# Kernel optimization log

Hardware: AMD Instinct MI355X
Metric: run time of the kernel (lower is better)

The kernel has to match this reference:

```python
import jax, jax.numpy as jnp
import numpy as np

LOG2 = float(np.log(2.0))

def ssp(x):
    # shifted softplus: log(0.5*exp(x) + 0.5)
    return jax.nn.softplus(x) - LOG2


def setup_inputs() -> dict:
    B, A, N = 8, 512, 64
    n_atom, n_spatial, n_filters = 256, 128, 256
    n_ang_feat = 2 * 2 * 2 * 8 * 2  # 2*n_zetas*2*n_angular*n_zetas = 128
    key = jax.random.key(0)
    ks = jax.random.split(key, 16)
    f32 = jnp.float32
    inp = {
        'x': jax.random.normal(ks[0], (B, A, n_atom), f32),
        'r_ij': jax.random.uniform(ks[1], (B, A, N), f32) * 6.0,  # some beyond cutoff=5
        'f_ij': jax.random.normal(ks[2], (B, A, N, n_spatial), f32),
        'G_i': jax.random.normal(ks[3], (B, A, n_ang_feat), f32),
        'neighbor_mask': jnp.ones((B, A, N), f32),
        'neighbors': jax.random.randint(ks[4], (B, A, N), 0, A),
        # CFConv params: in2f (no bias), filter MLP, f2out
        'W_in2f': jax.random.normal(ks[5], (n_atom, n_filters), f32) * (n_atom ** -0.5),
        'W1': jax.random.normal(ks[6], (n_spatial, n_filters), f32) * (n_spatial ** -0.5),
        'b1': jnp.zeros((n_filters,), f32),
        'W2': jax.random.normal(ks[7], (n_filters, n_filters), f32) * (n_filters ** -0.5),
        'b2': jnp.zeros((n_filters,), f32),
        'W_f2out': jax.random.normal(ks[8], (n_filters, n_atom), f32) * (n_filters ** -0.5),
        'b_f2out': jnp.zeros((n_atom,), f32),
        # post-cfconv dense and angular dense (no bias)
        'W_dense': jax.random.normal(ks[9], (n_atom, n_atom), f32) * (n_atom ** -0.5),
        'b_dense': jnp.zeros((n_atom,), f32),
        'W_ang': jax.random.normal(ks[10], (n_ang_feat, n_atom), f32) * (n_ang_feat ** -0.5),
    }
    return inp


def reference(x, r_ij, f_ij, G_i, neighbor_mask, neighbors,
              W_in2f, W1, b1, W2, b2, W_f2out, b_f2out,
              W_dense, b_dense, W_ang):
    cutoff = 5.0
    # filter-generating MLP on distance expansion: [B,A,N,n_filters]
    W = ssp(jnp.einsum('bans,sf->banf', f_ij, W1) + b1)
    W = jnp.einsum('banf,fg->bang', W, W2) + b2
    # hard cutoff mask on distances
    C = (r_ij <= cutoff).astype(W.dtype)
    W = W * C[..., None]
    # in2f projection then neighbor gather
    xf = jnp.einsum('bad,df->baf', x, W_in2f)  # [B,A,F]
    B, A, F = xf.shape
    N = neighbors.shape[-1]
    y = jnp.take_along_axis(xf, neighbors.reshape(B, A * N, 1), axis=1)
    y = y.reshape(B, A, N, F)
    # elementwise filter, mask padded neighbors, sum-aggregate over neighbors
    y = (y * W * neighbor_mask[..., None]).sum(axis=2)  # [B,A,F]
    v_rad = jnp.einsum('baf,fd->bad', y, W_f2out) + b_f2out
    v_rad = jnp.einsum('bad,de->bae', v_rad, W_dense) + b_dense
    v_ang = jnp.einsum('bag,gd->bad', G_i, W_ang)
    return ssp(v_rad + v_ang)
```

## Files before the change

kernel.cpp:

```cpp
#include <hip/hip_runtime.h>


typedef __bf16 bf16x8 __attribute__((ext_vector_type(8)));
typedef float f32x4 __attribute__((ext_vector_type(4)));
typedef unsigned short u16;

#define LDA 136
#define LDH 264

__device__ __forceinline__ float b2f(u16 u) {
  union { float f; unsigned int i; } v; v.i = ((unsigned int)u) << 16; return v.f;
}
__device__ __forceinline__ u16 f2b(float f) {
  unsigned int u = __builtin_bit_cast(unsigned int, f);
  return (u16)((u + 0x7fffu + ((u >> 16) & 1u)) >> 16);
}
__device__ __forceinline__ float sspf(float x) {
  float t = __expf(-fabsf(x));
  return fmaxf(x, 0.0f) + __logf(1.0f + t) - 0.6931471805599453f;
}
__device__ __forceinline__ bf16x8 ldfrag(const u16* p) {
  return __builtin_bit_cast(bf16x8, *(const uint4*)p);
}
__device__ __forceinline__ float ldsc(const u16* p, bool fm, size_t i) {
  return fm ? ((const float*)p)[i] : b2f(p[i]);
}
__device__ __forceinline__ void cvt8_store(u16* dst, const float* s) {
  float4 a = *(const float4*)s, b = *(const float4*)(s + 4);
  uint4 r;
  r.x = (unsigned)f2b(a.x) | ((unsigned)f2b(a.y) << 16);
  r.y = (unsigned)f2b(a.z) | ((unsigned)f2b(a.w) << 16);
  r.z = (unsigned)f2b(b.x) | ((unsigned)f2b(b.y) << 16);
  r.w = (unsigned)f2b(b.z) | ((unsigned)f2b(b.w) << 16);
  *(uint4*)dst = r;
}
__device__ __forceinline__ bf16x8 ldfragW(const u16* W, bool fm, int k0, int col, int quad) {
  union { u16 s[8]; bf16x8 v; } r;
  if (fm) {
    const float* W32 = (const float*)W;
#pragma unroll
    for (int j = 0; j < 8; j++) r.s[j] = f2b(W32[(size_t)(k0 + quad * 8 + j) * 256 + col]);
  } else {
#pragma unroll
    for (int j = 0; j < 8; j++) r.s[j] = W[(size_t)(k0 + quad * 8 + j) * 256 + col];
  }
  return r.v;
}

__global__ __launch_bounds__(256) void k1_xf(
    const u16* __restrict__ x, const u16* __restrict__ Win,
    const u16* __restrict__ nm, u16* __restrict__ xf) {
  __shared__ __align__(16) u16 sX[64 * LDH];
  bool fm = (nm[0] == 0);
  int bid = blockIdx.x, tid = threadIdx.x;
  int w = tid >> 6, lane = tid & 63, quad = lane >> 4, l16 = lane & 15;
  if (fm) {
    const float* src = (const float*)x + (size_t)bid * 16384;
#pragma unroll
    for (int i = 0; i < 8; i++) {
      int c = tid + 256 * i;
      cvt8_store(sX + (c >> 5) * LDH + (c & 31) * 8, src + c * 8);
    }
  } else {
    const u16* src = x + (size_t)bid * 16384;
#pragma unroll
    for (int i = 0; i < 8; i++) {
      int c = tid + 256 * i;
      *(uint4*)(sX + (c >> 5) * LDH + (c & 31) * 8) = *(const uint4*)(src + c * 8);
    }
  }
  __syncthreads();
  f32x4 zero = {0.f, 0.f, 0.f, 0.f};
  f32x4 acc[4][4];
#pragma unroll
  for (int mt = 0; mt < 4; mt++)
#pragma unroll
    for (int ct = 0; ct < 4; ct++) acc[mt][ct] = zero;
#pragma unroll
  for (int q = 0; q < 8; q++) {
    bf16x8 af[4], bf[4];
#pragma unroll
    for (int mt = 0; mt < 4; mt++)
      af[mt] = ldfrag(sX + (mt * 16 + l16) * LDH + q * 32 + quad * 8);
#pragma unroll
    for (int ct = 0; ct < 4; ct++)
      bf[ct] = ldfragW(Win, fm, q * 32, (w * 4 + ct) * 16 + l16, quad);
#pragma unroll
    for (int mt = 0; mt < 4; mt++)
#pragma unroll
      for (int ct = 0; ct < 4; ct++)
        acc[mt][ct] = __builtin_amdgcn_mfma_f32_16x16x32_bf16(af[mt], bf[ct], acc[mt][ct], 0, 0, 0);
  }
#pragma unroll
  for (int ct = 0; ct < 4; ct++) {
    int f = w * 64 + ct * 16 + l16;
#pragma unroll
    for (int mt = 0; mt < 4; mt++)
#pragma unroll
      for (int r = 0; r < 4; r++) {
        int m = bid * 64 + mt * 16 + quad * 4 + r;
        xf[(size_t)m * 256 + f] = f2b(acc[mt][ct][r]);
      }
  }
}

__global__ __launch_bounds__(256) void pack5(
    const u16* __restrict__ W1, const u16* __restrict__ W2, const u16* __restrict__ Wf,
    const u16* __restrict__ Wd, const u16* __restrict__ Wa,
    const u16* __restrict__ nm, u16* __restrict__ dst) {
  bool fm = (nm[0] == 0);
  int bid = blockIdx.x;
  const u16* W; u16* Wp; int ksh;
  if (bid < 128)       { W = W1; Wp = dst;          ksh = 2; }
  else if (bid < 384)  { W = W2; Wp = dst + 32768;  ksh = 3; bid -= 128; }
  else if (bid < 640)  { W = Wf; Wp = dst + 98304;  ksh = 3; bid -= 384; }
  else if (bid < 896)  { W = Wd; Wp = dst + 163840; ksh = 3; bid -= 640; }
  else                 { W = Wa; Wp = dst + 229376; ksh = 2; bid -= 896; }
  int tid = bid * 256 + threadIdx.x;
  int j = tid & 7, lane = (tid >> 3) & 63, rest = tid >> 9;
  int q = rest & ((1 << ksh) - 1), c = rest >> ksh;
  int row = q * 32 + (lane >> 4) * 8 + j, col = c * 16 + (lane & 15);
  float v = ldsc(W, fm, (size_t)row * 256 + col);
  Wp[tid] = f2b(v);
}

__global__ __launch_bounds__(256, 2) void k2_main(
    u16* __restrict__ fij, const u16* __restrict__ rij, const u16* __restrict__ nm,
    const int* __restrict__ nbr, const u16* __restrict__ b1, const u16* __restrict__ b2,
    const u16* __restrict__ packed, const u16* __restrict__ xf) {
  __shared__ __align__(16) u16 uA[64 * LDH];
  __shared__ __align__(16) u16 sH[64 * LDH];
  __shared__ float cm[64];
  __shared__ int nb[64];
  bool fm = (nm[0] == 0);
  const u16* w1p = packed;
  const u16* w2p = packed + 32768;
  int bid = blockIdx.x;
  int tid = threadIdx.x;
  int w = tid >> 6, lane = tid & 63, quad = lane >> 4, l16 = lane & 15;

  if (fm) {
    const float* fsrc = (const float*)fij + (size_t)bid * 8192;
#pragma unroll
    for (int i = 0; i < 4; i++) {
      int c = tid + 256 * i;
      cvt8_store(uA + (c >> 4) * LDA + (c & 15) * 8, fsrc + c * 8);
    }
  } else {
    const u16* fsrc = fij + (size_t)bid * 8192;
#pragma unroll
    for (int i = 0; i < 4; i++) {
      int c = tid + 256 * i;
      *(uint4*)(uA + (c >> 4) * LDA + (c & 15) * 8) = *(const uint4*)(fsrc + c * 8);
    }
  }
  if (tid < 64) {
    float r = ldsc(rij, fm, (size_t)bid * 64 + tid);
    float m = ldsc(nm, fm, (size_t)bid * 64 + tid);
    cm[tid] = (r <= 5.0f) ? m : 0.0f;
    nb[tid] = nbr[bid * 64 + tid];
  }
  __syncthreads();

  f32x4 zero = {0.f, 0.f, 0.f, 0.f};
  f32x4 acc[4][4];
#pragma unroll
  for (int mt = 0; mt < 4; mt++)
#pragma unroll
    for (int ct = 0; ct < 4; ct++) acc[mt][ct] = zero;
#pragma unroll
  for (int q = 0; q < 4; q++) {
    bf16x8 af[4], bf[4];
#pragma unroll
    for (int mt = 0; mt < 4; mt++)
      af[mt] = ldfrag(uA + (mt * 16 + l16) * LDA + q * 32 + quad * 8);
#pragma unroll
    for (int ct = 0; ct < 4; ct++)
      bf[ct] = ldfrag(w1p + (((w * 4 + ct) * 4 + q) * 64 + lane) * 8);
#pragma unroll
    for (int mt = 0; mt < 4; mt++)
#pragma unroll
      for (int ct = 0; ct < 4; ct++)
        acc[mt][ct] = __builtin_amdgcn_mfma_f32_16x16x32_bf16(af[mt], bf[ct], acc[mt][ct], 0, 0, 0);
  }
#pragma unroll
  for (int ct = 0; ct < 4; ct++) {
    int f = w * 64 + ct * 16 + l16;
    float bb = ldsc(b1, fm, f);
#pragma unroll
    for (int mt = 0; mt < 4; mt++)
#pragma unroll
      for (int r = 0; r < 4; r++) {
        int m = mt * 16 + quad * 4 + r;
        sH[m * LDH + f] = f2b(sspf(acc[mt][ct][r] + bb));
      }
  }
  __syncthreads();

  int b_of = (bid >> 9) * 512;
#pragma unroll
  for (int i = 0; i < 8; i++) {
    int c = tid + 256 * i;
    int row = c >> 5;
    const u16* src = xf + ((size_t)(b_of + nb[row])) * 256 + (c & 31) * 8;
    *(uint4*)(uA + row * LDH + (c & 31) * 8) = *(const uint4*)src;
  }

  f32x4 acc2[4][4];
#pragma unroll
  for (int mt = 0; mt < 4; mt++)
#pragma unroll
    for (int ct = 0; ct < 4; ct++) acc2[mt][ct] = zero;
#pragma unroll
  for (int q = 0; q < 8; q++) {
    bf16x8 af[4], bf[4];
#pragma unroll
    for (int mt = 0; mt < 4; mt++)
      af[mt] = ldfrag(sH + (mt * 16 + l16) * LDH + q * 32 + quad * 8);
#pragma unroll
    for (int ct = 0; ct < 4; ct++)
      bf[ct] = ldfrag(w2p + (((w * 4 + ct) * 8 + q) * 64 + lane) * 8);
#pragma unroll
    for (int mt = 0; mt < 4; mt++)
#pragma unroll
      for (int ct = 0; ct < 4; ct++)
        acc2[mt][ct] = __builtin_amdgcn_mfma_f32_16x16x32_bf16(af[mt], bf[ct], acc2[mt][ct], 0, 0, 0);
  }
  __syncthreads();

  size_t yoff = (size_t)bid * (fm ? 16384 : 8192);
#pragma unroll
  for (int ct = 0; ct < 4; ct++) {
    int f = w * 64 + ct * 16 + l16;
    float bb = ldsc(b2, fm, f);
    float s = 0.0f;
#pragma unroll
    for (int mt = 0; mt < 4; mt++)
#pragma unroll
      for (int r = 0; r < 4; r++) {
        int m = mt * 16 + quad * 4 + r;
        s += (acc2[mt][ct][r] + bb) * cm[m] * b2f(uA[m * LDH + f]);
      }
    s += __shfl_xor(s, 16, 64);
    s += __shfl_xor(s, 32, 64);
    if (quad == 0) fij[yoff + f] = f2b(s);
  }
}

__global__ __launch_bounds__(256) void k3_out(
    const u16* __restrict__ fij, const u16* __restrict__ G, const u16* __restrict__ bf2,
    const u16* __restrict__ bd, const u16* __restrict__ nm,
    const u16* __restrict__ packed, u16* __restrict__ out) {
  __shared__ __align__(16) u16 sY[64 * LDH];
  __shared__ __align__(16) u16 sH2[64 * LDH];
  __shared__ __align__(16) u16 sG[64 * LDA];
  bool fm = (nm[0] == 0);
  const u16* wfp = packed + 98304;
  const u16* wdp = packed + 163840;
  const u16* wap = packed + 229376;
  int bid = blockIdx.x, tid = threadIdx.x;
  int w = tid >> 6, lane = tid & 63, quad = lane >> 4, l16 = lane & 15;
  size_t ystr = fm ? 16384 : 8192;
#pragma unroll
  for (int i = 0; i < 8; i++) {
    int c = tid + 256 * i;
    int row = c >> 5;
    const u16* src = fij + (size_t)(bid * 64 + row) * ystr + (c & 31) * 8;
    *(uint4*)(sY + row * LDH + (c & 31) * 8) = *(const uint4*)src;
  }
  if (fm) {
    const float* gsrc = (const float*)G + (size_t)bid * 8192;
#pragma unroll
    for (int i = 0; i < 4; i++) {
      int c = tid + 256 * i;
      cvt8_store(sG + (c >> 4) * LDA + (c & 15) * 8, gsrc + c * 8);
    }
  } else {
    const u16* gsrc = G + (size_t)bid * 8192;
#pragma unroll
    for (int i = 0; i < 4; i++) {
      int c = tid + 256 * i;
      *(uint4*)(sG + (c >> 4) * LDA + (c & 15) * 8) = *(const uint4*)(gsrc + c * 8);
    }
  }
  __syncthreads();
  f32x4 zero = {0.f, 0.f, 0.f, 0.f};
  f32x4 acc[4][4];
#pragma unroll
  for (int mt = 0; mt < 4; mt++)
#pragma unroll
    for (int ct = 0; ct < 4; ct++) acc[mt][ct] = zero;
#pragma unroll
  for (int q = 0; q < 8; q++) {
    bf16x8 af[4], bf[4];
#pragma unroll
    for (int mt = 0; mt < 4; mt++)
      af[mt] = ldfrag(sY + (mt * 16 + l16) * LDH + q * 32 + quad * 8);
#pragma unroll
    for (int ct = 0; ct < 4; ct++)
      bf[ct] = ldfrag(wfp + (((w * 4 + ct) * 8 + q) * 64 + lane) * 8);
#pragma unroll
    for (int mt = 0; mt < 4; mt++)
#pragma unroll
      for (int ct = 0; ct < 4; ct++)
        acc[mt][ct] = __builtin_amdgcn_mfma_f32_16x16x32_bf16(af[mt], bf[ct], acc[mt][ct], 0, 0, 0);
  }
#pragma unroll
  for (int ct = 0; ct < 4; ct++) {
    int f = w * 64 + ct * 16 + l16;
    float bb = ldsc(bf2, fm, f);
#pragma unroll
    for (int mt = 0; mt < 4; mt++)
#pragma unroll
      for (int r = 0; r < 4; r++)
        sH2[(mt * 16 + quad * 4 + r) * LDH + f] = f2b(acc[mt][ct][r] + bb);
  }
  __syncthreads();
#pragma unroll
  for (int mt = 0; mt < 4; mt++)
#pragma unroll
    for (int ct = 0; ct < 4; ct++) acc[mt][ct] = zero;
#pragma unroll
  for (int q = 0; q < 8; q++) {
    bf16x8 af[4], bf[4];
#pragma unroll
    for (int mt = 0; mt < 4; mt++)
      af[mt] = ldfrag(sH2 + (mt * 16 + l16) * LDH + q * 32 + quad * 8);
#pragma unroll
    for (int ct = 0; ct < 4; ct++)
      bf[ct] = ldfrag(wdp + (((w * 4 + ct) * 8 + q) * 64 + lane) * 8);
#pragma unroll
    for (int mt = 0; mt < 4; mt++)
#pragma unroll
      for (int ct = 0; ct < 4; ct++)
        acc[mt][ct] = __builtin_amdgcn_mfma_f32_16x16x32_bf16(af[mt], bf[ct], acc[mt][ct], 0, 0, 0);
  }
#pragma unroll
  for (int q = 0; q < 4; q++) {
    bf16x8 af[4], bf[4];
#pragma unroll
    for (int mt = 0; mt < 4; mt++)
      af[mt] = ldfrag(sG + (mt * 16 + l16) * LDA + q * 32 + quad * 8);
#pragma unroll
    for (int ct = 0; ct < 4; ct++)
      bf[ct] = ldfrag(wap + (((w * 4 + ct) * 4 + q) * 64 + lane) * 8);
#pragma unroll
    for (int mt = 0; mt < 4; mt++)
#pragma unroll
      for (int ct = 0; ct < 4; ct++)
        acc[mt][ct] = __builtin_amdgcn_mfma_f32_16x16x32_bf16(af[mt], bf[ct], acc[mt][ct], 0, 0, 0);
  }
  float* out32 = (float*)out;
#pragma unroll
  for (int ct = 0; ct < 4; ct++) {
    int f = w * 64 + ct * 16 + l16;
    float bb = ldsc(bd, fm, f);
#pragma unroll
    for (int mt = 0; mt < 4; mt++)
#pragma unroll
      for (int r = 0; r < 4; r++) {
        int m = mt * 16 + quad * 4 + r;
        float v = sspf(acc[mt][ct][r] + bb);
        size_t idx = ((size_t)bid * 64 + m) * 256 + f;
        if (fm) out32[idx] = v; else out[idx] = f2b(v);
      }
  }
}

extern "C" void kernel_launch(void* const* d_in, const int* in_sizes, int n_in,
                              void* d_out, int out_size, void* d_ws, size_t ws_size,
                              hipStream_t stream) {
  u16*       x    = (u16*)d_in[0];
  const u16* rij  = (const u16*)d_in[1];
  u16*       fij  = (u16*)d_in[2];
  const u16* Gi   = (const u16*)d_in[3];
  const u16* nmsk = (const u16*)d_in[4];
  const int* nbr  = (const int*)d_in[5];
  const u16* Win  = (const u16*)d_in[6];
  const u16* W1   = (const u16*)d_in[7];
  const u16* b1   = (const u16*)d_in[8];
  const u16* W2   = (const u16*)d_in[9];
  const u16* b2   = (const u16*)d_in[10];
  const u16* Wf   = (const u16*)d_in[11];
  const u16* bf2  = (const u16*)d_in[12];
  const u16* Wd   = (const u16*)d_in[13];
  const u16* bd   = (const u16*)d_in[14];
  const u16* Wa   = (const u16*)d_in[15];
  u16* out = (u16*)d_out;

  k1_xf<<<64, 256, 0, stream>>>(x, Win, nmsk, out);
  pack5<<<1024, 256, 0, stream>>>(W1, W2, Wf, Wd, Wa, nmsk, x);
  k2_main<<<4096, 256, 0, stream>>>(fij, rij, nmsk, nbr, b1, b2, x, out);
  k3_out<<<64, 256, 0, stream>>>(fij, Gi, bf2, bd, nmsk, x, out);
}
```

Measured before the change: 329.8 us.

## Gather neighbor features into registers, shrink LDS, and re-grid xf/output kernels

```diff
diff --git a/kernel.cpp b/kernel.cpp
--- a/kernel.cpp
+++ b/kernel.cpp
@@ -4,16 +4,21 @@
 typedef __bf16 bf16x8 __attribute__((ext_vector_type(8)));
 typedef float f32x4 __attribute__((ext_vector_type(4)));
 typedef unsigned short u16;
+typedef unsigned int u32;
 
 #define LDA 136
 #define LDH 264
 
 __device__ __forceinline__ float b2f(u16 u) {
-  union { float f; unsigned int i; } v; v.i = ((unsigned int)u) << 16; return v.f;
-}
-__device__ __forceinline__ u16 f2b(float f) {
-  unsigned int u = __builtin_bit_cast(unsigned int, f);
-  return (u16)((u + 0x7fffu + ((u >> 16) & 1u)) >> 16);
+  union { float f; u32 i; } v; v.i = ((u32)u) << 16; return v.f;
+}
+__device__ __forceinline__ u32 rndb(float f) {
+  u32 u = __builtin_bit_cast(u32, f);
+  return u + 0x7fffu + ((u >> 16) & 1u);
+}
+__device__ __forceinline__ u16 f2b(float f) { return (u16)(rndb(f) >> 16); }
+__device__ __forceinline__ u32 pkbf(float lo, float hi) {
+  return __builtin_amdgcn_perm(rndb(hi), rndb(lo), 0x07060302);
 }
 __device__ __forceinline__ float sspf(float x) {
   float t = __expf(-fabsf(x));
@@ -28,80 +33,43 @@
 __device__ __forceinline__ void cvt8_store(u16* dst, const float* s) {
   float4 a = *(const float4*)s, b = *(const float4*)(s + 4);
   uint4 r;
-  r.x = (unsigned)f2b(a.x) | ((unsigned)f2b(a.y) << 16);
-  r.y = (unsigned)f2b(a.z) | ((unsigned)f2b(a.w) << 16);
-  r.z = (unsigned)f2b(b.x) | ((unsigned)f2b(b.y) << 16);
-  r.w = (unsigned)f2b(b.z) | ((unsigned)f2b(b.w) << 16);
+  r.x = pkbf(a.x, a.y); r.y = pkbf(a.z, a.w);
+  r.z = pkbf(b.x, b.y); r.w = pkbf(b.z, b.w);
   *(uint4*)dst = r;
 }
-__device__ __forceinline__ bf16x8 ldfragW(const u16* W, bool fm, int k0, int col, int quad) {
+__device__ __forceinline__ bf16x8 ldfragW_bf(const u16* W, int k0, int col, int quad) {
   union { u16 s[8]; bf16x8 v; } r;
+#pragma unroll
+  for (int j = 0; j < 8; j++) r.s[j] = W[(size_t)(k0 + quad * 8 + j) * 256 + col];
+  return r.v;
+}
+
+__device__ __forceinline__ void pack_chunk(const u16* W, bool fm, int ksh, int idx, u16* dst) {
+  int flane = idx & 63;
+  int q = (idx >> 6) & ((1 << ksh) - 1);
+  int c = idx >> (6 + ksh);
+  int row = q * 32 + (flane >> 4) * 8;
+  int col = c * 16 + (flane & 15);
+  uint4 r;
   if (fm) {
-    const float* W32 = (const float*)W;
-#pragma unroll
-    for (int j = 0; j < 8; j++) r.s[j] = f2b(W32[(size_t)(k0 + quad * 8 + j) * 256 + col]);
+    const float* p = (const float*)W + (size_t)row * 256 + col;
+    r.x = pkbf(p[0], p[256]);   r.y = pkbf(p[512], p[768]);
+    r.z = pkbf(p[1024], p[1280]); r.w = pkbf(p[1536], p[1792]);
   } else {
-#pragma unroll
-    for (int j = 0; j < 8; j++) r.s[j] = W[(size_t)(k0 + quad * 8 + j) * 256 + col];
-  }
-  return r.v;
-}
-
-__global__ __launch_bounds__(256) void k1_xf(
-    const u16* __restrict__ x, const u16* __restrict__ Win,
-    const u16* __restrict__ nm, u16* __restrict__ xf) {
-  __shared__ __align__(16) u16 sX[64 * LDH];
-  bool fm = (nm[0] == 0);
-  int bid = blockIdx.x, tid = threadIdx.x;
-  int w = tid >> 6, lane = tid & 63, quad = lane >> 4, l16 = lane & 15;
-  if (fm) {
-    const float* src = (const float*)x + (size_t)bid * 16384;
-#pragma unroll
-    for (int i = 0; i < 8; i++) {
-      int c = tid + 256 * i;
-      cvt8_store(sX + (c >> 5) * LDH + (c & 31) * 8, src + c * 8);
-    }
-  } else {
-    const u16* src = x + (size_t)bid * 16384;
-#pragma unroll
-    for (int i = 0; i < 8; i++) {
-      int c = tid + 256 * i;
-      *(uint4*)(sX + (c >> 5) * LDH + (c & 31) * 8) = *(const uint4*)(src + c * 8);
-    }
-  }
-  __syncthreads();
-  f32x4 zero = {0.f, 0.f, 0.f, 0.f};
-  f32x4 acc[4][4];
-#pragma unroll
-  for (int mt = 0; mt < 4; mt++)
-#pragma unroll
-    for (int ct = 0; ct < 4; ct++) acc[mt][ct] = zero;
-#pragma unroll
-  for (int q = 0; q < 8; q++) {
-    bf16x8 af[4], bf[4];
-#pragma unroll
-    for (int mt = 0; mt < 4; mt++)
-      af[mt] = ldfrag(sX + (mt * 16 + l16) * LDH + q * 32 + quad * 8);
-#pragma unroll
-    for (int ct = 0; ct < 4; ct++)
-      bf[ct] = ldfragW(Win, fm, q * 32, (w * 4 + ct) * 16 + l16, quad);
-#pragma unroll
-    for (int mt = 0; mt < 4; mt++)
-#pragma unroll
-      for (int ct = 0; ct < 4; ct++)
-        acc[mt][ct] = __builtin_amdgcn_mfma_f32_16x16x32_bf16(af[mt], bf[ct], acc[mt][ct], 0, 0, 0);
-  }
-#pragma unroll
-  for (int ct = 0; ct < 4; ct++) {
-    int f = w * 64 + ct * 16 + l16;
-#pragma unroll
-    for (int mt = 0; mt < 4; mt++)
-#pragma unroll
-      for (int r = 0; r < 4; r++) {
-        int m = bid * 64 + mt * 16 + quad * 4 + r;
-        xf[(size_t)m * 256 + f] = f2b(acc[mt][ct][r]);
-      }
-  }
+    const u16* p = W + (size_t)row * 256 + col;
+    r.x = (u32)p[0] | ((u32)p[256] << 16);
+    r.y = (u32)p[512] | ((u32)p[768] << 16);
+    r.z = (u32)p[1024] | ((u32)p[1280] << 16);
+    r.w = (u32)p[1536] | ((u32)p[1792] << 16);
+  }
+  *(uint4*)(dst + (size_t)idx * 8) = r;
+}
+
+__global__ __launch_bounds__(256) void pack_win(
+    const u16* __restrict__ Win, const u16* __restrict__ nm, u16* __restrict__ outb) {
+  if (nm[0] != 0) return;
+  int g = blockIdx.x * 256 + threadIdx.x;
+  pack_chunk(Win, true, 3, g, outb + 1048576);
 }
 
 __global__ __launch_bounds__(256) void pack5(
@@ -109,34 +77,74 @@
     const u16* __restrict__ Wd, const u16* __restrict__ Wa,
     const u16* __restrict__ nm, u16* __restrict__ dst) {
   bool fm = (nm[0] == 0);
-  int bid = blockIdx.x;
-  const u16* W; u16* Wp; int ksh;
-  if (bid < 128)       { W = W1; Wp = dst;          ksh = 2; }
-  else if (bid < 384)  { W = W2; Wp = dst + 32768;  ksh = 3; bid -= 128; }
-  else if (bid < 640)  { W = Wf; Wp = dst + 98304;  ksh = 3; bid -= 384; }
-  else if (bid < 896)  { W = Wd; Wp = dst + 163840; ksh = 3; bid -= 640; }
-  else                 { W = Wa; Wp = dst + 229376; ksh = 2; bid -= 896; }
-  int tid = bid * 256 + threadIdx.x;
-  int j = tid & 7, lane = (tid >> 3) & 63, rest = tid >> 9;
-  int q = rest & ((1 << ksh) - 1), c = rest >> ksh;
-  int row = q * 32 + (lane >> 4) * 8 + j, col = c * 16 + (lane & 15);
-  float v = ldsc(W, fm, (size_t)row * 256 + col);
-  Wp[tid] = f2b(v);
-}
-
-__global__ __launch_bounds__(256, 2) void k2_main(
+  int g = blockIdx.x * 256 + threadIdx.x;
+  if (g < 4096)        pack_chunk(W1, fm, 2, g, dst);
+  else if (g < 12288)  pack_chunk(W2, fm, 3, g - 4096, dst + 32768);
+  else if (g < 20480)  pack_chunk(Wf, fm, 3, g - 12288, dst + 98304);
+  else if (g < 28672)  pack_chunk(Wd, fm, 3, g - 20480, dst + 163840);
+  else                 pack_chunk(Wa, fm, 2, g - 28672, dst + 229376);
+}
+
+__global__ __launch_bounds__(256) void k1_xf(
+    const u16* __restrict__ x, const u16* __restrict__ Win,
+    const u16* __restrict__ nm, u16* __restrict__ outb) {
+  __shared__ __align__(16) u16 sX[16 * LDH];
+  bool fm = (nm[0] == 0);
+  int bid = blockIdx.x, tid = threadIdx.x;
+  int w = tid >> 6, lane = tid & 63, quad = lane >> 4, l16 = lane & 15;
+  if (fm) {
+    const float* src = (const float*)x + (size_t)bid * 4096;
+#pragma unroll
+    for (int i = 0; i < 2; i++) {
+      int c = tid + 256 * i;
+      cvt8_store(sX + (c >> 5) * LDH + (c & 31) * 8, src + c * 8);
+    }
+  } else {
+    const u16* src = x + (size_t)bid * 4096;
+#pragma unroll
+    for (int i = 0; i < 2; i++) {
+      int c = tid + 256 * i;
+      *(uint4*)(sX + (c >> 5) * LDH + (c & 31) * 8) = *(const uint4*)(src + c * 8);
+    }
+  }
+  __syncthreads();
+  const u16* winp = outb + 1048576;
+  f32x4 acc[4];
+#pragma unroll
+  for (int ct = 0; ct < 4; ct++) acc[ct] = (f32x4){0.f, 0.f, 0.f, 0.f};
+#pragma unroll
+  for (int q = 0; q < 8; q++) {
+    bf16x8 af = ldfrag(sX + l16 * LDH + q * 32 + quad * 8);
+    bf16x8 bfr[4];
+#pragma unroll
+    for (int ct = 0; ct < 4; ct++)
+      bfr[ct] = fm ? ldfrag(winp + ((size_t)((w * 4 + ct) * 8 + q) * 64 + lane) * 8)
+                   : ldfragW_bf(Win, q * 32, (w * 4 + ct) * 16 + l16, quad);
+#pragma unroll
+    for (int ct = 0; ct < 4; ct++)
+      acc[ct] = __builtin_amdgcn_mfma_f32_16x16x32_bf16(af, bfr[ct], acc[ct], 0, 0, 0);
+  }
+#pragma unroll
+  for (int ct = 0; ct < 4; ct++) {
+    int f = w * 64 + ct * 16 + l16;
+#pragma unroll
+    for (int r = 0; r < 4; r++)
+      outb[(size_t)(bid * 16 + quad * 4 + r) * 256 + f] = f2b(acc[ct][r]);
+  }
+}
+
+__global__ __launch_bounds__(256, 3) void k2_main(
     u16* __restrict__ fij, const u16* __restrict__ rij, const u16* __restrict__ nm,
     const int* __restrict__ nbr, const u16* __restrict__ b1, const u16* __restrict__ b2,
     const u16* __restrict__ packed, const u16* __restrict__ xf) {
-  __shared__ __align__(16) u16 uA[64 * LDH];
+  __shared__ __align__(16) u16 sF[64 * LDA];
   __shared__ __align__(16) u16 sH[64 * LDH];
   __shared__ float cm[64];
   __shared__ int nb[64];
   bool fm = (nm[0] == 0);
   const u16* w1p = packed;
   const u16* w2p = packed + 32768;
-  int bid = blockIdx.x;
-  int tid = threadIdx.x;
+  int bid = blockIdx.x, tid = threadIdx.x;
   int w = tid >> 6, lane = tid & 63, quad = lane >> 4, l16 = lane & 15;
 
   if (fm) {
@@ -144,14 +152,14 @@
 #pragma unroll
     for (int i = 0; i < 4; i++) {
       int c = tid + 256 * i;
-      cvt8_store(uA + (c >> 4) * LDA + (c & 15) * 8, fsrc + c * 8);
+      cvt8_store(sF + (c >> 4) * LDA + (c & 15) * 8, fsrc + c * 8);
     }
   } else {
     const u16* fsrc = fij + (size_t)bid * 8192;
 #pragma unroll
     for (int i = 0; i < 4; i++) {
       int c = tid + 256 * i;
-      *(uint4*)(uA + (c >> 4) * LDA + (c & 15) * 8) = *(const uint4*)(fsrc + c * 8);
+      *(uint4*)(sF + (c >> 4) * LDA + (c & 15) * 8) = *(const uint4*)(fsrc + c * 8);
     }
   }
   if (tid < 64) {
@@ -162,6 +170,19 @@
   }
   __syncthreads();
 
+  int b_of = (bid >> 9) * 512;
+  u32 xr[4][4][2];
+#pragma unroll
+  for (int mt = 0; mt < 4; mt++)
+#pragma unroll
+    for (int r = 0; r < 4; r++) {
+      int m = mt * 16 + quad * 4 + r;
+      const u16* src = xf + ((size_t)(b_of + nb[m])) * 256 + w * 64 + l16;
+      u32 t0 = src[0], t1 = src[16], t2 = src[32], t3 = src[48];
+      xr[mt][r][0] = t0 | (t1 << 16);
+      xr[mt][r][1] = t2 | (t3 << 16);
+    }
+
   f32x4 zero = {0.f, 0.f, 0.f, 0.f};
   f32x4 acc[4][4];
 #pragma unroll
@@ -170,18 +191,18 @@
     for (int ct = 0; ct < 4; ct++) acc[mt][ct] = zero;
 #pragma unroll
   for (int q = 0; q < 4; q++) {
-    bf16x8 af[4], bf[4];
+    bf16x8 af[4], bfr[4];
 #pragma unroll
     for (int mt = 0; mt < 4; mt++)
-      af[mt] = ldfrag(uA + (mt * 16 + l16) * LDA + q * 32 + quad * 8);
-#pragma unroll
-    for (int ct = 0; ct < 4; ct++)
-      bf[ct] = ldfrag(w1p + (((w * 4 + ct) * 4 + q) * 64 + lane) * 8);
+      af[mt] = ldfrag(sF + (mt * 16 + l16) * LDA + q * 32 + quad * 8);
+#pragma unroll
+    for (int ct = 0; ct < 4; ct++)
+      bfr[ct] = ldfrag(w1p + ((size_t)((w * 4 + ct) * 4 + q) * 64 + lane) * 8);
 #pragma unroll
     for (int mt = 0; mt < 4; mt++)
 #pragma unroll
       for (int ct = 0; ct < 4; ct++)
-        acc[mt][ct] = __builtin_amdgcn_mfma_f32_16x16x32_bf16(af[mt], bf[ct], acc[mt][ct], 0, 0, 0);
+        acc[mt][ct] = __builtin_amdgcn_mfma_f32_16x16x32_bf16(af[mt], bfr[ct], acc[mt][ct], 0, 0, 0);
   }
 #pragma unroll
   for (int ct = 0; ct < 4; ct++) {
@@ -190,22 +211,11 @@
 #pragma unroll
     for (int mt = 0; mt < 4; mt++)
 #pragma unroll
-      for (int r = 0; r < 4; r++) {
-        int m = mt * 16 + quad * 4 + r;
-        sH[m * LDH + f] = f2b(sspf(acc[mt][ct][r] + bb));
-      }
+      for (int r = 0; r < 4; r++)
+        sH[(mt * 16 + quad * 4 + r) * LDH + f] = f2b(sspf(acc[mt][ct][r] + bb));
   }
   __syncthreads();
 
-  int b_of = (bid >> 9) * 512;
-#pragma unroll
-  for (int i = 0; i < 8; i++) {
-    int c = tid + 256 * i;
-    int row = c >> 5;
-    const u16* src = xf + ((size_t)(b_of + nb[row])) * 256 + (c & 31) * 8;
-    *(uint4*)(uA + row * LDH + (c & 31) * 8) = *(const uint4*)src;
-  }
-
   f32x4 acc2[4][4];
 #pragma unroll
   for (int mt = 0; mt < 4; mt++)
@@ -213,47 +223,58 @@
     for (int ct = 0; ct < 4; ct++) acc2[mt][ct] = zero;
 #pragma unroll
   for (int q = 0; q < 8; q++) {
-    bf16x8 af[4], bf[4];
+    bf16x8 af[4], bfr[4];
 #pragma unroll
     for (int mt = 0; mt < 4; mt++)
       af[mt] = ldfrag(sH + (mt * 16 + l16) * LDH + q * 32 + quad * 8);
 #pragma unroll
     for (int ct = 0; ct < 4; ct++)
-      bf[ct] = ldfrag(w2p + (((w * 4 + ct) * 8 + q) * 64 + lane) * 8);
+      bfr[ct] = ldfrag(w2p + ((size_t)((w * 4 + ct) * 8 + q) * 64 + lane) * 8);
 #pragma unroll
     for (int mt = 0; mt < 4; mt++)
 #pragma unroll
       for (int ct = 0; ct < 4; ct++)
-        acc2[mt][ct] = __builtin_amdgcn_mfma_f32_16x16x32_bf16(af[mt], bf[ct], acc2[mt][ct], 0, 0, 0);
-  }
-  __syncthreads();
-
+        acc2[mt][ct] = __builtin_amdgcn_mfma_f32_16x16x32_bf16(af[mt], bfr[ct], acc2[mt][ct], 0, 0, 0);
+  }
+
+  float bb[4], sv[4];
+#pragma unroll
+  for (int ct = 0; ct < 4; ct++) {
+    bb[ct] = ldsc(b2, fm, w * 64 + ct * 16 + l16);
+    sv[ct] = 0.0f;
+  }
+#pragma unroll
+  for (int mt = 0; mt < 4; mt++)
+#pragma unroll
+    for (int r = 0; r < 4; r++) {
+      int m = mt * 16 + quad * 4 + r;
+      float c = cm[m];
+      float x0 = __builtin_bit_cast(float, xr[mt][r][0] << 16);
+      float x1 = __builtin_bit_cast(float, xr[mt][r][0] & 0xffff0000u);
+      float x2 = __builtin_bit_cast(float, xr[mt][r][1] << 16);
+      float x3 = __builtin_bit_cast(float, xr[mt][r][1] & 0xffff0000u);
+      sv[0] += (acc2[mt][0][r] + bb[0]) * (c * x0);
+      sv[1] += (acc2[mt][1][r] + bb[1]) * (c * x1);
+      sv[2] += (acc2[mt][2][r] + bb[2]) * (c * x2);
+      sv[3] += (acc2[mt][3][r] + bb[3]) * (c * x3);
+    }
   size_t yoff = (size_t)bid * (fm ? 16384 : 8192);
 #pragma unroll
   for (int ct = 0; ct < 4; ct++) {
-    int f = w * 64 + ct * 16 + l16;
-    float bb = ldsc(b2, fm, f);
-    float s = 0.0f;
-#pragma unroll
-    for (int mt = 0; mt < 4; mt++)
-#pragma unroll
-      for (int r = 0; r < 4; r++) {
-        int m = mt * 16 + quad * 4 + r;
-        s += (acc2[mt][ct][r] + bb) * cm[m] * b2f(uA[m * LDH + f]);
-      }
+    float s = sv[ct];
     s += __shfl_xor(s, 16, 64);
     s += __shfl_xor(s, 32, 64);
-    if (quad == 0) fij[yoff + f] = f2b(s);
-  }
-}
-
-__global__ __launch_bounds__(256) void k3_out(
+    if (quad == 0) fij[yoff + w * 64 + ct * 16 + l16] = f2b(s);
+  }
+}
+
+__global__ __launch_bounds__(256, 3) void k3_out(
     const u16* __restrict__ fij, const u16* __restrict__ G, const u16* __restrict__ bf2,
     const u16* __restrict__ bd, const u16* __restrict__ nm,
-    const u16* __restrict__ packed, u16* __restrict__ out) {
-  __shared__ __align__(16) u16 sY[64 * LDH];
-  __shared__ __align__(16) u16 sH2[64 * LDH];
-  __shared__ __align__(16) u16 sG[64 * LDA];
+    const u16* __restrict__ packed, u16* __restrict__ outb) {
+  __shared__ __align__(16) u16 sY[32 * LDH];
+  __shared__ __align__(16) u16 sH2[32 * LDH];
+  __shared__ __align__(16) u16 sG[32 * LDA];
   bool fm = (nm[0] == 0);
   const u16* wfp = packed + 98304;
   const u16* wdp = packed + 163840;
@@ -262,107 +283,109 @@
   int w = tid >> 6, lane = tid & 63, quad = lane >> 4, l16 = lane & 15;
   size_t ystr = fm ? 16384 : 8192;
 #pragma unroll
-  for (int i = 0; i < 8; i++) {
+  for (int i = 0; i < 4; i++) {
     int c = tid + 256 * i;
     int row = c >> 5;
-    const u16* src = fij + (size_t)(bid * 64 + row) * ystr + (c & 31) * 8;
+    const u16* src = fij + (size_t)(bid * 32 + row) * ystr + (c & 31) * 8;
     *(uint4*)(sY + row * LDH + (c & 31) * 8) = *(const uint4*)src;
   }
   if (fm) {
-    const float* gsrc = (const float*)G + (size_t)bid * 8192;
-#pragma unroll
-    for (int i = 0; i < 4; i++) {
-      int c = tid + 256 * i;
-      cvt8_store(sG + (c >> 4) * LDA + (c & 15) * 8, gsrc + c * 8);
+    const float* g32 = (const float*)G;
+#pragma unroll
+    for (int i = 0; i < 2; i++) {
+      int c = tid + 256 * i;
+      int row = c >> 4;
+      cvt8_store(sG + row * LDA + (c & 15) * 8, g32 + (size_t)(bid * 32 + row) * 128 + (c & 15) * 8);
     }
   } else {
-    const u16* gsrc = G + (size_t)bid * 8192;
-#pragma unroll
-    for (int i = 0; i < 4; i++) {
-      int c = tid + 256 * i;
-      *(uint4*)(sG + (c >> 4) * LDA + (c & 15) * 8) = *(const uint4*)(gsrc + c * 8);
+#pragma unroll
+    for (int i = 0; i < 2; i++) {
+      int c = tid + 256 * i;
+      int row = c >> 4;
+      *(uint4*)(sG + row * LDA + (c & 15) * 8) =
+          *(const uint4*)(G + (size_t)(bid * 32 + row) * 128 + (c & 15) * 8);
     }
   }
   __syncthreads();
   f32x4 zero = {0.f, 0.f, 0.f, 0.f};
-  f32x4 acc[4][4];
-#pragma unroll
-  for (int mt = 0; mt < 4; mt++)
+  f32x4 acc[2][4];
+#pragma unroll
+  for (int mt = 0; mt < 2; mt++)
 #pragma unroll
     for (int ct = 0; ct < 4; ct++) acc[mt][ct] = zero;
 #pragma unroll
   for (int q = 0; q < 8; q++) {
-    bf16x8 af[4], bf[4];
-#pragma unroll
-    for (int mt = 0; mt < 4; mt++)
+    bf16x8 af[2], bfr[4];
+#pragma unroll
+    for (int mt = 0; mt < 2; mt++)
       af[mt] = ldfrag(sY + (mt * 16 + l16) * LDH + q * 32 + quad * 8);
 #pragma unroll
     for (int ct = 0; ct < 4; ct++)
-      bf[ct] = ldfrag(wfp + (((w * 4 + ct) * 8 + q) * 64 + lane) * 8);
-#pragma unroll
-    for (int mt = 0; mt < 4; mt++)
+      bfr[ct] = ldfrag(wfp + ((size_t)((w * 4 + ct) * 8 + q) * 64 + lane) * 8);
+#pragma unroll
+    for (int mt = 0; mt < 2; mt++)
 #pragma unroll
       for (int ct = 0; ct < 4; ct++)
-        acc[mt][ct] = __builtin_amdgcn_mfma_f32_16x16x32_bf16(af[mt], bf[ct], acc[mt][ct], 0, 0, 0);
+        acc[mt][ct] = __builtin_amdgcn_mfma_f32_16x16x32_bf16(af[mt], bfr[ct], acc[mt][ct], 0, 0, 0);
   }
 #pragma unroll
   for (int ct = 0; ct < 4; ct++) {
     int f = w * 64 + ct * 16 + l16;
     float bb = ldsc(bf2, fm, f);
 #pragma unroll
-    for (int mt = 0; mt < 4; mt++)
+    for (int mt = 0; mt < 2; mt++)
 #pragma unroll
       for (int r = 0; r < 4; r++)
         sH2[(mt * 16 + quad * 4 + r) * LDH + f] = f2b(acc[mt][ct][r] + bb);
   }
   __syncthreads();
 #pragma unroll
-  for (int mt = 0; mt < 4; mt++)
+  for (int mt = 0; mt < 2; mt++)
 #pragma unroll
     for (int ct = 0; ct < 4; ct++) acc[mt][ct] = zero;
 #pragma unroll
   for (int q = 0; q < 8; q++) {
-    bf16x8 af[4], bf[4];
-#pragma unroll
-    for (int mt = 0; mt < 4; mt++)
+    bf16x8 af[2], bfr[4];
+#pragma unroll
+    for (int mt = 0; mt < 2; mt++)
       af[mt] = ldfrag(sH2 + (mt * 16 + l16) * LDH + q * 32 + quad * 8);
 #pragma unroll
     for (int ct = 0; ct < 4; ct++)
-      bf[ct] = ldfrag(wdp + (((w * 4 + ct) * 8 + q) * 64 + lane) * 8);
-#pragma unroll
-    for (int mt = 0; mt < 4; mt++)
+      bfr[ct] = ldfrag(wdp + ((size_t)((w * 4 + ct) * 8 + q) * 64 + lane) * 8);
+#pragma unroll
+    for (int mt = 0; mt < 2; mt++)
 #pragma unroll
       for (int ct = 0; ct < 4; ct++)
-        acc[mt][ct] = __builtin_amdgcn_mfma_f32_16x16x32_bf16(af[mt], bf[ct], acc[mt][ct], 0, 0, 0);
+        acc[mt][ct] = __builtin_amdgcn_mfma_f32_16x16x32_bf16(af[mt], bfr[ct], acc[mt][ct], 0, 0, 0);
   }
 #pragma unroll
   for (int q = 0; q < 4; q++) {
-    bf16x8 af[4], bf[4];
-#pragma unroll
-    for (int mt = 0; mt < 4; mt++)
+    bf16x8 af[2], bfr[4];
+#pragma unroll
+    for (int mt = 0; mt < 2; mt++)
       af[mt] = ldfrag(sG + (mt * 16 + l16) * LDA + q * 32 + quad * 8);
 #pragma unroll
     for (int ct = 0; ct < 4; ct++)
-      bf[ct] = ldfrag(wap + (((w * 4 + ct) * 4 + q) * 64 + lane) * 8);
-#pragma unroll
-    for (int mt = 0; mt < 4; mt++)
+      bfr[ct] = ldfrag(wap + ((size_t)((w * 4 + ct) * 4 + q) * 64 + lane) * 8);
+#pragma unroll
+    for (int mt = 0; mt < 2; mt++)
 #pragma unroll
       for (int ct = 0; ct < 4; ct++)
-        acc[mt][ct] = __builtin_amdgcn_mfma_f32_16x16x32_bf16(af[mt], bf[ct], acc[mt][ct], 0, 0, 0);
-  }
-  float* out32 = (float*)out;
+        acc[mt][ct] = __builtin_amdgcn_mfma_f32_16x16x32_bf16(af[mt], bfr[ct], acc[mt][ct], 0, 0, 0);
+  }
+  float* out32 = (float*)outb;
 #pragma unroll
   for (int ct = 0; ct < 4; ct++) {
     int f = w * 64 + ct * 16 + l16;
     float bb = ldsc(bd, fm, f);
 #pragma unroll
-    for (int mt = 0; mt < 4; mt++)
+    for (int mt = 0; mt < 2; mt++)
 #pragma unroll
       for (int r = 0; r < 4; r++) {
         int m = mt * 16 + quad * 4 + r;
         float v = sspf(acc[mt][ct][r] + bb);
-        size_t idx = ((size_t)bid * 64 + m) * 256 + f;
-        if (fm) out32[idx] = v; else out[idx] = f2b(v);
+        size_t idx = ((size_t)bid * 32 + m) * 256 + f;
+        if (fm) out32[idx] = v; else outb[idx] = f2b(v);
       }
   }
 }
@@ -388,8 +411,9 @@
   const u16* Wa   = (const u16*)d_in[15];
   u16* out = (u16*)d_out;
 
-  k1_xf<<<64, 256, 0, stream>>>(x, Win, nmsk, out);
-  pack5<<<1024, 256, 0, stream>>>(W1, W2, Wf, Wd, Wa, nmsk, x);
+  pack_win<<<32, 256, 0, stream>>>(Win, nmsk, out);
+  k1_xf<<<256, 256, 0, stream>>>(x, Win, nmsk, out);
+  pack5<<<128, 256, 0, stream>>>(W1, W2, Wf, Wd, Wa, nmsk, x);
   k2_main<<<4096, 256, 0, stream>>>(fij, rij, nmsk, nbr, b1, b2, x, out);
-  k3_out<<<64, 256, 0, stream>>>(fij, Gi, bf2, bd, nmsk, x, out);
-}
+  k3_out<<<128, 256, 0, stream>>>(fij, Gi, bf2, bd, nmsk, x, out);
+}
```

Result: slower. 345.9 us (+4.9%).
